# Optimization experiments

Measured on AMD Instinct MI355X. Metric: run time of the kernel, lower is better.

## Reference

```python
import jax, jax.numpy as jnp
import numpy as np

B, T, D, U, C = 256, 512, 128, 128, 64


def setup_inputs() -> dict:
    key = jax.random.key(0)
    ks = jax.random.split(key, 4)
    s_in = 1.0 / np.sqrt(D)
    s_u = 1.0 / np.sqrt(U)
    return {
        "inputs": jax.random.normal(ks[0], (B, T, D), dtype=jnp.float32),
        "W1": jax.random.normal(ks[1], (D, U), dtype=jnp.float32) * s_in,
        "b1": jnp.zeros((U,), dtype=jnp.float32),
        "W2": jax.random.normal(ks[2], (U, U), dtype=jnp.float32) * s_u,
        "b2": jnp.zeros((U,), dtype=jnp.float32),
        "Wc": jax.random.normal(ks[3], (U, C), dtype=jnp.float32) * s_u,
        "bc": jnp.zeros((C,), dtype=jnp.float32),
    }


def reference(inputs, W1, b1, W2, b2, Wc, bc):
    # state_{t} = tanh(x_t @ W1 + b1) + tanh(state_{t-1} @ W2 + b2)
    # Input projection has no recurrent dependency -> precompute in one big GEMM.
    h = jnp.tanh(jnp.einsum("btd,du->btu", inputs, W1) + b1)  # (B, T, U)

    def step(state, h_t):
        y = h_t + jnp.tanh(state @ W2 + b2)  # (B, U)
        return y, y

    state0 = jnp.zeros((inputs.shape[0], W2.shape[0]), dtype=inputs.dtype)
    _, ys = jax.lax.scan(step, state0, jnp.swapaxes(h, 0, 1))  # ys: (T, B, U)
    features = jnp.swapaxes(ys, 0, 1)  # (B, T, U)
    # classifier: Dense head applied to stacked features
    return jnp.einsum("btu,uc->btc", features, Wc) + bc
```

## Files before the change

### kernel.cpp

```cpp
#include <hip/hip_runtime.h>

#define NB 256
#define NT 512
#define ND 128
#define NU 128
#define NC 64
#define NM (NB * NT)
#define YP 136
#define SCL 2.8853900817779268f

typedef _Float16 half2v __attribute__((ext_vector_type(2)));
typedef _Float16 half4v __attribute__((ext_vector_type(4)));
typedef _Float16 half8v __attribute__((ext_vector_type(8)));
typedef float f32x4 __attribute__((ext_vector_type(4)));
typedef float v2f __attribute__((ext_vector_type(2)));

#define MFMA(a, b, c) __builtin_amdgcn_mfma_f32_16x16x32_f16((a), (b), (c), 0, 0, 0)

__device__ __forceinline__ half2v pk2(float a, float b) {
  return __builtin_bit_cast(half2v, __builtin_amdgcn_cvt_pkrtz(a, b));
}

__device__ __forceinline__ float tanh_s(float s) {
  float e = __builtin_amdgcn_exp2f(s);
  return fmaf(-2.0f, __builtin_amdgcn_rcpf(e + 1.0f), 1.0f);
}
__device__ __forceinline__ float ym1(float s, float th) {
  float e = __builtin_amdgcn_exp2f(s);
  return fmaf(-2.0f, __builtin_amdgcn_rcpf(e + 1.0f), th);
}

__device__ __forceinline__ void wg_barrier() {
  asm volatile("s_waitcnt lgkmcnt(0)\n\ts_barrier" ::: "memory");
}

__global__ __launch_bounds__(256, 1) void k1_inproj(
    const float* __restrict__ x, const float* __restrict__ W1,
    const float* __restrict__ b1v, _Float16* __restrict__ TH)
{
  __shared__ _Float16 W1T[ND * YP];
  const int tid = (int)threadIdx.x;
  for (int i = tid; i < ND * NU / 2; i += 256) {
    int n = i & 127, kh = i >> 7;
    half2v p = {(_Float16)(SCL * W1[(size_t)(2 * kh) * NU + n]),
                (_Float16)(SCL * W1[(size_t)(2 * kh + 1) * NU + n])};
    *(half2v*)&W1T[n * YP + 2 * kh] = p;
  }
  __syncthreads();

  const int L = tid & 63, wv = tid >> 6;
  const int v = L & 15, q = L >> 4;
  const int m0 = (int)blockIdx.x * 64 + wv * 16;

  const float* xr = x + (size_t)(m0 + v) * ND + 8 * q;
  half8v xf[4];
#pragma unroll
  for (int kk = 0; kk < 4; ++kk) {
    float4 a = *(const float4*)(xr + 32 * kk);
    float4 b = *(const float4*)(xr + 32 * kk + 4);
    half2v p0 = pk2(a.x, a.y), p1 = pk2(a.z, a.w);
    half2v p2 = pk2(b.x, b.y), p3 = pk2(b.z, b.w);
    xf[kk] = (half8v){p0[0], p0[1], p1[0], p1[1], p2[0], p2[1], p3[0], p3[1]};
  }

#pragma unroll
  for (int ht = 0; ht < 8; ++ht) {
    f32x4 acc;
    {
      float4 bb = *(const float4*)&b1v[16 * ht + 4 * q];
      acc = (f32x4){SCL * bb.x, SCL * bb.y, SCL * bb.z, SCL * bb.w};
    }
#pragma unroll
    for (int kk = 0; kk < 4; ++kk) {
      half8v wa = *(const half8v*)&W1T[(16 * ht + v) * YP + 32 * kk + 8 * q];
      acc = MFMA(wa, xf[kk], acc);
    }
    half2v zlo = pk2(tanh_s(acc[0]), tanh_s(acc[1]));
    half2v zhi = pk2(tanh_s(acc[2]), tanh_s(acc[3]));
    half4v z = {zlo[0], zlo[1], zhi[0], zhi[1]};
    *(half4v*)&TH[(size_t)(m0 + v) * NU + 16 * ht + 4 * q] = z;
  }
}

__global__ __launch_bounds__(256, 1) void k2_recur(
    const _Float16* __restrict__ TH, const float* __restrict__ W2,
    const float* __restrict__ b2v, _Float16* __restrict__ Yws)
{
  __shared__ _Float16 Ybuf[2][16 * YP];

  const int tid = (int)threadIdx.x;
  const int w = tid >> 6;
  const int L = tid & 63;
  const int v = L & 15, q = L >> 4;
  const int b0 = (int)blockIdx.x * 16;
  const _Float16* rd = &Ybuf[0][0] + v * YP + 8 * q;
  const f32x4 zero4 = (f32x4){0.f, 0.f, 0.f, 0.f};

  half8v w2f[2][4];
#pragma unroll
  for (int ht = 0; ht < 2; ++ht)
#pragma unroll
    for (int kk = 0; kk < 4; ++kk) {
      half8v h;
#pragma unroll
      for (int j = 0; j < 8; ++j)
        h[j] = (_Float16)(SCL *
               W2[(size_t)(32 * kk + 8 * q + j) * NU + 32 * w + 16 * ht + v]);
      w2f[ht][kk] = h;
    }
  f32x4 racc[2], b2f[2];
#pragma unroll
  for (int ht = 0; ht < 2; ++ht) {
    const int h0 = 32 * w + 16 * ht + 4 * q;
    float4 bb = *(const float4*)&b2v[h0];
    racc[ht] = (f32x4){SCL * bb.x, SCL * bb.y, SCL * bb.z, SCL * bb.w};
    f32x4 cs = zero4;
#pragma unroll 4
    for (int k = 0; k < NU; ++k) {
      float4 ww = *(const float4*)&W2[(size_t)k * NU + h0];
      cs += (f32x4){ww.x, ww.y, ww.z, ww.w};
    }
    b2f[ht] = racc[ht] +
              (f32x4){SCL * cs[0], SCL * cs[1], SCL * cs[2], SCL * cs[3]};
  }

  const _Float16* thp = TH + ((size_t)(b0 + v) * NT) * NU + 32 * w + 4 * q;
  _Float16* yp = Yws + ((size_t)(b0 + v) * NT) * NU + 32 * w + 4 * q;
  _Float16* wr = &Ybuf[0][0] + v * YP + 32 * w + 4 * q;
  const half4v one4 = {(_Float16)1.f, (_Float16)1.f, (_Float16)1.f, (_Float16)1.f};

#define LOADTH(R_, T_)                                                        \
  {                                                                           \
    const _Float16* p_ = thp + (size_t)(T_) * NU;                             \
    R_[0] = *(const half4v*)(p_);                                             \
    R_[1] = *(const half4v*)(p_ + 16);                                        \
  }

  half4v rg0[2], rg1[2], rg2[2], rg3[2];
  LOADTH(rg0, 0) LOADTH(rg1, 1) LOADTH(rg2, 2) LOADTH(rg3, 3)

#define RSTEP(T_, R_, BUF_)                                                   \
  {                                                                           \
    _Pragma("unroll")                                                         \
    for (int ht = 0; ht < 2; ++ht) {                                          \
      half4v t4 = R_[ht];                                                     \
      half2v ylo = pk2(ym1(racc[ht][0], (float)t4[0]),                        \
                       ym1(racc[ht][1], (float)t4[1]));                       \
      half2v yhi = pk2(ym1(racc[ht][2], (float)t4[2]),                        \
                       ym1(racc[ht][3], (float)t4[3]));                       \
      half4v y4 = {ylo[0], ylo[1], yhi[0], yhi[1]};                           \
      *(half4v*)(wr + (BUF_) * (16 * YP) + 16 * ht) = y4;                     \
      *(half4v*)(yp + (size_t)(T_) * NU + 16 * ht) = y4 + one4;               \
    }                                                                         \
    {                                                                         \
      int tn = (T_) + 4; tn = tn < NT ? tn : NT - 1;                          \
      LOADTH(R_, tn)                                                          \
    }                                                                         \
    wg_barrier();                                                             \
    {                                                                         \
      half8v yf0 = *(const half8v*)(rd + (BUF_) * (16 * YP) + 0);             \
      half8v yf1 = *(const half8v*)(rd + (BUF_) * (16 * YP) + 32);            \
      half8v yf2 = *(const half8v*)(rd + (BUF_) * (16 * YP) + 64);            \
      half8v yf3 = *(const half8v*)(rd + (BUF_) * (16 * YP) + 96);            \
      _Pragma("unroll")                                                       \
      for (int ht = 0; ht < 2; ++ht) {                                        \
        f32x4 ra = MFMA(w2f[ht][0], yf0, b2f[ht]);                            \
        f32x4 rb = MFMA(w2f[ht][1], yf1, zero4);                              \
        ra = MFMA(w2f[ht][2], yf2, ra);                                       \
        rb = MFMA(w2f[ht][3], yf3, rb);                                       \
        racc[ht] = ra + rb;                                                   \
      }                                                                       \
    }                                                                         \
  }

#pragma unroll 1
  for (int t = 0; t < NT; t += 4) {
    RSTEP(t + 0, rg0, 0)
    RSTEP(t + 1, rg1, 1)
    RSTEP(t + 2, rg2, 0)
    RSTEP(t + 3, rg3, 1)
  }
#undef RSTEP
#undef LOADTH
}

__global__ __launch_bounds__(256, 1) void k3_head(
    const _Float16* __restrict__ Y, const float* __restrict__ Wc,
    const float* __restrict__ bcv, float* __restrict__ out)
{
  __shared__ _Float16 WcT[NC * YP];
  const int tid = (int)threadIdx.x;
  for (int i = tid; i < NU * NC; i += 256) {
    int k = i >> 6, c = i & 63;
    WcT[c * YP + k] = (_Float16)Wc[i];
  }
  __syncthreads();

  const int L = tid & 63, wv = tid >> 6;
  const int v = L & 15, q = L >> 4;
  const int m0 = (int)blockIdx.x * 64 + wv * 16;

  const _Float16* yr = Y + (size_t)(m0 + v) * NU + 8 * q;
  half8v yf[4];
#pragma unroll
  for (int kk = 0; kk < 4; ++kk) yf[kk] = *(const half8v*)(yr + 32 * kk);

  float* op = out + (size_t)(m0 + v) * NC + 4 * q;
#pragma unroll
  for (int ct = 0; ct < 4; ++ct) {
    f32x4 acc;
    {
      float4 bb = *(const float4*)&bcv[16 * ct + 4 * q];
      acc = (f32x4){bb.x, bb.y, bb.z, bb.w};
    }
#pragma unroll
    for (int kk = 0; kk < 4; ++kk) {
      half8v wa = *(const half8v*)&WcT[(16 * ct + v) * YP + 32 * kk + 8 * q];
      acc = MFMA(wa, yf[kk], acc);
    }
    *(float4*)(op + 16 * ct) = (float4){acc[0], acc[1], acc[2], acc[3]};
  }
}

__device__ __forceinline__ float fast_tanh(float x) {
  float e = __expf(2.0f * x);
  return 1.0f - 2.0f / (e + 1.0f);
}
__device__ __forceinline__ float bcast(float val, int i) {
  return __builtin_bit_cast(float, __builtin_amdgcn_readlane(__builtin_bit_cast(int, val), i));
}

__global__ __launch_bounds__(256, 1) void rnn_fallback(
    const float* __restrict__ x, const float* __restrict__ W1,
    const float* __restrict__ b1v, const float* __restrict__ W2,
    const float* __restrict__ b2v, const float* __restrict__ Wc,
    const float* __restrict__ bcv, float* __restrict__ out)
{
  __shared__ float xring[16][ND];
  __shared__ float pH[2][4][NU];
  __shared__ float pR[2][4][NU];
  __shared__ float pC[2][4][NC];

  const int tid  = (int)threadIdx.x;
  const int lane = tid & 63;
  const int kg   = tid >> 6;
  const int b    = (int)blockIdx.x;
  const float4* xr4 = (const float4*)(x + (size_t)b * NT * ND);

  v2f w1f[32], w2f[32];
  float wcf[32];
#pragma unroll
  for (int i = 0; i < 32; ++i) {
    int k = kg * 32 + i;
    w1f[i] = (v2f){W1[k * NU + lane], W1[k * NU + lane + 64]};
    w2f[i] = (v2f){W2[k * NU + lane], W2[k * NU + lane + 64]};
    wcf[i] = Wc[k * NC + lane];
  }
  const float biasc = bcv[lane];
  float bias1 = 0.f, bias2 = 0.f;
  if (lane < 32) { bias1 = b1v[kg * 32 + lane]; bias2 = b2v[kg * 32 + lane]; }

  float4 stg = make_float4(0.f, 0.f, 0.f, 0.f);
  if (lane < 32) {
    float4 a0 = xr4[(kg + 0) * 32 + lane];
    float4 a1 = xr4[(kg + 4) * 32 + lane];
    ((float4*)xring[kg + 0])[lane] = a0;
    ((float4*)xring[kg + 4])[lane] = a1;
    stg = xr4[(kg + 8) * 32 + lane];
  }
  float yseg = 0.f;
  wg_barrier();

  for (int t = 0; t < NT; ++t) {
    const int pb = t & 1;
    v2f accH0 = {0.f, 0.f}, accH1 = {0.f, 0.f};
    const float4* xb = (const float4*)&xring[t & 15][kg * 32];
#pragma unroll
    for (int i = 0; i < 4; ++i) {
      float4 xa = xb[2 * i];
      float4 xc = xb[2 * i + 1];
      accH0 = w1f[8*i+0] * (v2f){xa.x, xa.x} + accH0;
      accH1 = w1f[8*i+1] * (v2f){xa.y, xa.y} + accH1;
      accH0 = w1f[8*i+2] * (v2f){xa.z, xa.z} + accH0;
      accH1 = w1f[8*i+3] * (v2f){xa.w, xa.w} + accH1;
      accH0 = w1f[8*i+4] * (v2f){xc.x, xc.x} + accH0;
      accH1 = w1f[8*i+5] * (v2f){xc.y, xc.y} + accH1;
      accH0 = w1f[8*i+6] * (v2f){xc.z, xc.z} + accH0;
      accH1 = w1f[8*i+7] * (v2f){xc.w, xc.w} + accH1;
    }
    v2f accH = accH0 + accH1;
    v2f accR0 = {0.f, 0.f}, accR1 = {0.f, 0.f};
    float accC0 = 0.f, accC1 = 0.f;
#pragma unroll
    for (int i = 0; i < 16; ++i) {
      float s0 = bcast(yseg, 2 * i);
      float s1 = bcast(yseg, 2 * i + 1);
      accR0 = w2f[2*i+0] * (v2f){s0, s0} + accR0;
      accR1 = w2f[2*i+1] * (v2f){s1, s1} + accR1;
      accC0 = fmaf(s0, wcf[2*i+0], accC0);
      accC1 = fmaf(s1, wcf[2*i+1], accC1);
    }
    v2f accR = accR0 + accR1;
    float accC = accC0 + accC1;

    pH[pb][kg][lane]      = accH.x;
    pH[pb][kg][lane + 64] = accH.y;
    pR[pb][kg][lane]      = accR.x;
    pR[pb][kg][lane + 64] = accR.y;
    pC[pb][kg][lane]      = accC;

    if (kg == (t & 3)) {
      if (lane < 32) {
        ((float4*)xring[(t + 8) & 15])[lane] = stg;
        int r = t + 12; r = (r < NT) ? r : (NT - 1);
        stg = xr4[r * 32 + lane];
      }
    }
    wg_barrier();
    if (lane < 32) {
      const int j = kg * 32 + lane;
      float hs = bias1, rs = bias2;
#pragma unroll
      for (int g = 0; g < 4; ++g) { hs += pH[pb][g][j]; rs += pR[pb][g][j]; }
      yseg = fast_tanh(hs) + fast_tanh(rs);
    }
    if (kg == ((t + 2) & 3) && t >= 1) {
      float cs = biasc;
#pragma unroll
      for (int g = 0; g < 4; ++g) cs += pC[pb][g][lane];
      out[((size_t)b * NT + (t - 1)) * NC + lane] = cs;
    }
  }
  float accC0 = 0.f, accC1 = 0.f;
#pragma unroll
  for (int i = 0; i < 16; ++i) {
    float s0 = bcast(yseg, 2 * i);
    float s1 = bcast(yseg, 2 * i + 1);
    accC0 = fmaf(s0, wcf[2*i+0], accC0);
    accC1 = fmaf(s1, wcf[2*i+1], accC1);
  }
  pC[0][kg][lane] = accC0 + accC1;
  wg_barrier();
  if (kg == 0) {
    float cs = biasc;
#pragma unroll
    for (int g = 0; g < 4; ++g) cs += pC[0][g][lane];
    out[((size_t)b * NT + (NT - 1)) * NC + lane] = cs;
  }
}

extern "C" void kernel_launch(void* const* d_in, const int* in_sizes, int n_in,
                              void* d_out, int out_size, void* d_ws, size_t ws_size,
                              hipStream_t stream) {
  (void)in_sizes; (void)n_in; (void)out_size;
  const float* x   = (const float*)d_in[0];
  const float* W1  = (const float*)d_in[1];
  const float* b1v = (const float*)d_in[2];
  const float* W2  = (const float*)d_in[3];
  const float* b2v = (const float*)d_in[4];
  const float* Wc  = (const float*)d_in[5];
  const float* bcv = (const float*)d_in[6];
  float* out = (float*)d_out;

  const size_t need = (size_t)NM * NU * 2 * 2;
  if (ws_size >= need) {
    _Float16* TH = (_Float16*)d_ws;
    _Float16* Yw = TH + (size_t)NM * NU;
    hipLaunchKernelGGL(k1_inproj, dim3(NM / 64), dim3(256), 0, stream, x, W1, b1v, TH);
    hipLaunchKernelGGL(k2_recur, dim3(NB / 16), dim3(256), 0, stream, TH, W2, b2v, Yw);
    hipLaunchKernelGGL(k3_head, dim3(NM / 64), dim3(256), 0, stream, Yw, Wc, bcv, out);
  } else {
    hipLaunchKernelGGL(rnn_fallback, dim3(NB), dim3(256), 0, stream,
                       x, W1, b1v, W2, b2v, Wc, bcv, out);
  }
}
```

Baseline: 341.1 us.

## Run recurrence in a single wavefront per block to drop workgroup barriers

The recurrent kernel now uses one 64-lane wavefront per 16-row batch tile instead of four waves. Each wave holds all of W2 in registers (8x4 fragments) and exchanges the new state through LDS with only a waitcnt, so the per-step s_barrier goes away. The layout of the TH intermediate is permuted so each lane loads contiguous 8-wide chunks. The +1 offset stored in Y is moved into a column-sum bias in the head kernel. The cost is higher register pressure and a serial MFMA chain of 32 per step on a single wave per CU, with only 16 blocks occupying the GPU.

```diff
diff --git a/kernel.cpp b/kernel.cpp
--- a/kernel.cpp
+++ b/kernel.cpp
@@ -36,7 +36,7 @@
 
 __global__ __launch_bounds__(256, 1) void k1_inproj(
     const float* __restrict__ x, const float* __restrict__ W1,
-    const float* __restrict__ b1v, _Float16* __restrict__ TH)
+    const float* __restrict__ b1v, _Float16* __restrict__ THp)
 {
   __shared__ _Float16 W1T[ND * YP];
   const int tid = (int)threadIdx.x;
@@ -78,129 +78,134 @@
     half2v zlo = pk2(tanh_s(acc[0]), tanh_s(acc[1]));
     half2v zhi = pk2(tanh_s(acc[2]), tanh_s(acc[3]));
     half4v z = {zlo[0], zlo[1], zhi[0], zhi[1]};
-    *(half4v*)&TH[(size_t)(m0 + v) * NU + 16 * ht + 4 * q] = z;
-  }
-}
-
-__global__ __launch_bounds__(256, 1) void k2_recur(
-    const _Float16* __restrict__ TH, const float* __restrict__ W2,
+    *(half4v*)&THp[(size_t)(m0 + v) * NU + 32 * q + 4 * ht] = z;
+  }
+}
+
+__global__ __launch_bounds__(64, 1) void k2_recur(
+    const _Float16* __restrict__ THp, const float* __restrict__ W2,
     const float* __restrict__ b2v, _Float16* __restrict__ Yws)
 {
-  __shared__ _Float16 Ybuf[2][16 * YP];
-
-  const int tid = (int)threadIdx.x;
-  const int w = tid >> 6;
-  const int L = tid & 63;
+  __shared__ _Float16 Ybuf[2][2048];
+  __shared__ float csb[NU];
+
+  const int L = (int)threadIdx.x & 63;
   const int v = L & 15, q = L >> 4;
   const int b0 = (int)blockIdx.x * 16;
-  const _Float16* rd = &Ybuf[0][0] + v * YP + 8 * q;
-  const f32x4 zero4 = (f32x4){0.f, 0.f, 0.f, 0.f};
-
-  half8v w2f[2][4];
-#pragma unroll
-  for (int ht = 0; ht < 2; ++ht)
+
+  half8v w2f[8][4];
+#pragma unroll
+  for (int ht = 0; ht < 8; ++ht)
 #pragma unroll
     for (int kk = 0; kk < 4; ++kk) {
       half8v h;
 #pragma unroll
       for (int j = 0; j < 8; ++j)
-        h[j] = (_Float16)(SCL *
-               W2[(size_t)(32 * kk + 8 * q + j) * NU + 32 * w + 16 * ht + v]);
+        h[j] = (_Float16)(SCL * W2[(size_t)(32 * kk + 8 * q + j) * NU + 16 * ht + v]);
       w2f[ht][kk] = h;
     }
-  f32x4 racc[2], b2f[2];
-#pragma unroll
-  for (int ht = 0; ht < 2; ++ht) {
-    const int h0 = 32 * w + 16 * ht + 4 * q;
+
+  {
+    float s0 = 0.f, s1 = 0.f;
+    for (int k = 0; k < NU; ++k) {
+      s0 += W2[(size_t)k * NU + L];
+      s1 += W2[(size_t)k * NU + L + 64];
+    }
+    csb[L] = s0;
+    csb[L + 64] = s1;
+    asm volatile("s_waitcnt lgkmcnt(0)" ::: "memory");
+  }
+
+  f32x4 rA[8], rB[8], b2f[8];
+#pragma unroll
+  for (int ht = 0; ht < 8; ++ht) {
+    const int h0 = 16 * ht + 4 * q;
     float4 bb = *(const float4*)&b2v[h0];
-    racc[ht] = (f32x4){SCL * bb.x, SCL * bb.y, SCL * bb.z, SCL * bb.w};
-    f32x4 cs = zero4;
-#pragma unroll 4
-    for (int k = 0; k < NU; ++k) {
-      float4 ww = *(const float4*)&W2[(size_t)k * NU + h0];
-      cs += (f32x4){ww.x, ww.y, ww.z, ww.w};
-    }
-    b2f[ht] = racc[ht] +
-              (f32x4){SCL * cs[0], SCL * cs[1], SCL * cs[2], SCL * cs[3]};
-  }
-
-  const _Float16* thp = TH + ((size_t)(b0 + v) * NT) * NU + 32 * w + 4 * q;
-  _Float16* yp = Yws + ((size_t)(b0 + v) * NT) * NU + 32 * w + 4 * q;
-  _Float16* wr = &Ybuf[0][0] + v * YP + 32 * w + 4 * q;
-  const half4v one4 = {(_Float16)1.f, (_Float16)1.f, (_Float16)1.f, (_Float16)1.f};
+    f32x4 cs4 = *(const f32x4*)&csb[h0];
+    rA[ht] = (f32x4){SCL * bb.x, SCL * bb.y, SCL * bb.z, SCL * bb.w};
+    b2f[ht] = rA[ht] + (f32x4){SCL * cs4[0], SCL * cs4[1], SCL * cs4[2], SCL * cs4[3]};
+  }
+
+  const _Float16* thp = THp + (size_t)(b0 + v) * NT * NU + 32 * q;
+  _Float16* ypb = Yws + (size_t)(b0 + v) * NT * NU + 8 * q;
+  _Float16* wr = &Ybuf[0][0] + v * 8 + 128 * (q >> 1) + 4 * (q & 1);
+  const _Float16* rd = &Ybuf[0][0] + L * 8;
 
 #define LOADTH(R_, T_)                                                        \
   {                                                                           \
     const _Float16* p_ = thp + (size_t)(T_) * NU;                             \
-    R_[0] = *(const half4v*)(p_);                                             \
-    R_[1] = *(const half4v*)(p_ + 16);                                        \
-  }
-
-  half4v rg0[2], rg1[2], rg2[2], rg3[2];
-  LOADTH(rg0, 0) LOADTH(rg1, 1) LOADTH(rg2, 2) LOADTH(rg3, 3)
-
-#define RSTEP(T_, R_, BUF_)                                                   \
+    R_[0] = *(const half8v*)(p_ + 0);                                         \
+    R_[1] = *(const half8v*)(p_ + 8);                                         \
+    R_[2] = *(const half8v*)(p_ + 16);                                        \
+    R_[3] = *(const half8v*)(p_ + 24);                                        \
+  }
+
+  half8v thr0[4], thr1[4], thr2[4], thr3[4];
+  LOADTH(thr0, 0) LOADTH(thr1, 1) LOADTH(thr2, 2) LOADTH(thr3, 3)
+
+#define RSTEP(T_, THR_, BUF_, RA_, RN_)                                       \
   {                                                                           \
     _Pragma("unroll")                                                         \
-    for (int ht = 0; ht < 2; ++ht) {                                          \
-      half4v t4 = R_[ht];                                                     \
-      half2v ylo = pk2(ym1(racc[ht][0], (float)t4[0]),                        \
-                       ym1(racc[ht][1], (float)t4[1]));                       \
-      half2v yhi = pk2(ym1(racc[ht][2], (float)t4[2]),                        \
-                       ym1(racc[ht][3], (float)t4[3]));                       \
-      half4v y4 = {ylo[0], ylo[1], yhi[0], yhi[1]};                           \
-      *(half4v*)(wr + (BUF_) * (16 * YP) + 16 * ht) = y4;                     \
-      *(half4v*)(yp + (size_t)(T_) * NU + 16 * ht) = y4 + one4;               \
+    for (int kk = 0; kk < 4; ++kk) {                                          \
+      _Pragma("unroll")                                                       \
+      for (int hh = 0; hh < 2; ++hh) {                                        \
+        const int ht = 2 * kk + hh;                                           \
+        const int j0 = 4 * hh;                                                \
+        half2v ylo = pk2(ym1(RA_[ht][0], (float)THR_[kk][j0 + 0]),            \
+                         ym1(RA_[ht][1], (float)THR_[kk][j0 + 1]));           \
+        half2v yhi = pk2(ym1(RA_[ht][2], (float)THR_[kk][j0 + 2]),            \
+                         ym1(RA_[ht][3], (float)THR_[kk][j0 + 3]));           \
+        half4v y4 = {ylo[0], ylo[1], yhi[0], yhi[1]};                         \
+        *(half4v*)(wr + (BUF_) * 2048 + kk * 512 + hh * 256) = y4;            \
+      }                                                                       \
+      asm volatile("s_waitcnt lgkmcnt(0)" ::: "memory");                      \
+      half8v yf = *(const half8v*)(rd + (BUF_) * 2048 + kk * 512);            \
+      *(half8v*)(ypb + (size_t)(T_) * NU + 32 * kk) = yf;                     \
+      _Pragma("unroll")                                                       \
+      for (int ht = 0; ht < 8; ++ht)                                          \
+        RN_[ht] = MFMA(w2f[ht][kk], yf, (kk == 0) ? b2f[ht] : RN_[ht]);       \
     }                                                                         \
     {                                                                         \
       int tn = (T_) + 4; tn = tn < NT ? tn : NT - 1;                          \
-      LOADTH(R_, tn)                                                          \
-    }                                                                         \
-    wg_barrier();                                                             \
-    {                                                                         \
-      half8v yf0 = *(const half8v*)(rd + (BUF_) * (16 * YP) + 0);             \
-      half8v yf1 = *(const half8v*)(rd + (BUF_) * (16 * YP) + 32);            \
-      half8v yf2 = *(const half8v*)(rd + (BUF_) * (16 * YP) + 64);            \
-      half8v yf3 = *(const half8v*)(rd + (BUF_) * (16 * YP) + 96);            \
-      _Pragma("unroll")                                                       \
-      for (int ht = 0; ht < 2; ++ht) {                                        \
-        f32x4 ra = MFMA(w2f[ht][0], yf0, b2f[ht]);                            \
-        f32x4 rb = MFMA(w2f[ht][1], yf1, zero4);                              \
-        ra = MFMA(w2f[ht][2], yf2, ra);                                       \
-        rb = MFMA(w2f[ht][3], yf3, rb);                                       \
-        racc[ht] = ra + rb;                                                   \
-      }                                                                       \
+      LOADTH(THR_, tn)                                                        \
     }                                                                         \
   }
 
 #pragma unroll 1
   for (int t = 0; t < NT; t += 4) {
-    RSTEP(t + 0, rg0, 0)
-    RSTEP(t + 1, rg1, 1)
-    RSTEP(t + 2, rg2, 0)
-    RSTEP(t + 3, rg3, 1)
+    RSTEP(t + 0, thr0, 0, rA, rB)
+    RSTEP(t + 1, thr1, 1, rB, rA)
+    RSTEP(t + 2, thr2, 0, rA, rB)
+    RSTEP(t + 3, thr3, 1, rB, rA)
   }
 #undef RSTEP
 #undef LOADTH
 }
 
 __global__ __launch_bounds__(256, 1) void k3_head(
-    const _Float16* __restrict__ Y, const float* __restrict__ Wc,
+    const _Float16* __restrict__ Yp, const float* __restrict__ Wc,
     const float* __restrict__ bcv, float* __restrict__ out)
 {
   __shared__ _Float16 WcT[NC * YP];
+  __shared__ float bcp[NC];
   const int tid = (int)threadIdx.x;
   for (int i = tid; i < NU * NC; i += 256) {
     int k = i >> 6, c = i & 63;
     WcT[c * YP + k] = (_Float16)Wc[i];
   }
   __syncthreads();
+  if (tid < NC) {
+    float s = 0.f;
+    for (int k = 0; k < NU; ++k) s += (float)WcT[tid * YP + k];
+    bcp[tid] = s;
+  }
+  __syncthreads();
 
   const int L = tid & 63, wv = tid >> 6;
   const int v = L & 15, q = L >> 4;
   const int m0 = (int)blockIdx.x * 64 + wv * 16;
 
-  const _Float16* yr = Y + (size_t)(m0 + v) * NU + 8 * q;
+  const _Float16* yr = Yp + (size_t)(m0 + v) * NU + 8 * q;
   half8v yf[4];
 #pragma unroll
   for (int kk = 0; kk < 4; ++kk) yf[kk] = *(const half8v*)(yr + 32 * kk);
@@ -211,7 +216,8 @@
     f32x4 acc;
     {
       float4 bb = *(const float4*)&bcv[16 * ct + 4 * q];
-      acc = (f32x4){bb.x, bb.y, bb.z, bb.w};
+      f32x4 cq = *(const f32x4*)&bcp[16 * ct + 4 * q];
+      acc = (f32x4){bb.x, bb.y, bb.z, bb.w} + cq;
     }
 #pragma unroll
     for (int kk = 0; kk < 4; ++kk) {
@@ -364,10 +370,10 @@
 
   const size_t need = (size_t)NM * NU * 2 * 2;
   if (ws_size >= need) {
-    _Float16* TH = (_Float16*)d_ws;
-    _Float16* Yw = TH + (size_t)NM * NU;
-    hipLaunchKernelGGL(k1_inproj, dim3(NM / 64), dim3(256), 0, stream, x, W1, b1v, TH);
-    hipLaunchKernelGGL(k2_recur, dim3(NB / 16), dim3(256), 0, stream, TH, W2, b2v, Yw);
+    _Float16* THp = (_Float16*)d_ws;
+    _Float16* Yw  = THp + (size_t)NM * NU;
+    hipLaunchKernelGGL(k1_inproj, dim3(NM / 64), dim3(256), 0, stream, x, W1, b1v, THp);
+    hipLaunchKernelGGL(k2_recur, dim3(NB / 16), dim3(64), 0, stream, THp, W2, b2v, Yw);
     hipLaunchKernelGGL(k3_head, dim3(NM / 64), dim3(256), 0, stream, Yw, Wc, bcv, out);
   } else {
     hipLaunchKernelGGL(rnn_fallback, dim3(NB), dim3(256), 0, stream,
```

After: 558.8 us. 63.8% more time.
